# Performance work log

Hardware: AMD Instinct MI355X
Metric: run time of the kernel (lower is better)

Reference implementation:

```python
import jax, jax.numpy as jnp
import numpy as np

E, B, T = 8, 8, 1024
DIN = 640    # hidden_state_dim + conf_dim
DH = 1024    # 2 * hidden_state_dim
DOUT = 128   # 1024 // num_experts (slicing=True)
CODE = 256
TAU = 0.1
IMPORTANCE_REG = 0.01
EPS = 1e-8


def setup_inputs() -> dict:
    key = jax.random.key(0)
    ks = jax.random.split(key, 9)
    h = jax.random.normal(ks[0], (B, T, DIN), jnp.float32)
    code_emb = jax.random.normal(ks[1], (B, T, CODE), jnp.float32)
    u = jax.random.uniform(ks[2], (B, T, E), jnp.float32, 1e-6, 1.0 - 1e-6)
    gumbel_noise = -jnp.log(-jnp.log(u))
    code_anchor = jax.random.normal(ks[3], (E, CODE), jnp.float32)
    feature_importance = jax.random.normal(ks[4], (E, DIN), jnp.float32)
    W1 = jax.random.normal(ks[5], (E, DIN, DH), jnp.float32) * 0.02
    b1 = jax.random.normal(ks[6], (E, DH), jnp.float32) * 0.02
    W2 = jax.random.normal(ks[7], (E, DH, DOUT), jnp.float32) * 0.02
    b2 = jax.random.normal(ks[8], (E, DOUT), jnp.float32) * 0.02
    return {"h": h, "code_emb": code_emb, "gumbel_noise": gumbel_noise,
            "code_anchor": code_anchor, "feature_importance": feature_importance,
            "W1": W1, "b1": b1, "W2": W2, "b2": b2}


def _l2norm(x, axis):
    n = jnp.sqrt(jnp.sum(x * x, axis=axis, keepdims=True))
    return x / jnp.maximum(n, 1e-12)


def reference(h, code_emb, gumbel_noise, code_anchor, feature_importance, W1, b1, W2, b2):
    # router logits: cosine similarity between code_emb and code anchors  [B,T,E]
    anchor_n = _l2norm(code_anchor, axis=1)
    code_n = _l2norm(code_emb, axis=-1)
    router_logits = jnp.einsum('btd,ed->bte', code_n, anchor_n)
    # gumbel-softmax, tau=0.1, hard=False (noise provided for determinism)
    expert_weights = jax.nn.softmax((router_logits + gumbel_noise) / TAU, axis=-1)  # [B,T,E]
    # temperature-scaled importance softmax; importance_temperature=0.5, clamp no-op
    temp = jnp.clip(jnp.float32(0.5), 0.1, 5.0)
    importance = jax.nn.softmax(feature_importance / temp, axis=1)  # [E,DIN]
    # per-expert importance-weighted inputs [B,E,T,DIN]
    weighted_h = h[:, None, :, :] * importance[None, :, None, :]
    # all experts as one batched 2-layer MLP (exact GELU like torch nn.GELU)
    hid = jax.nn.gelu(jnp.einsum('betd,edh->beth', weighted_h, W1) + b1[None, :, None, :],
                      approximate=False)
    expert_outputs = jnp.einsum('beth,eho->beto', hid, W2) + b2[None, :, None, :]  # [B,E,T,DOUT]
    # slicing combine: expert i fills output slice [i*DOUT:(i+1)*DOUT], scaled by its gate
    gated = expert_outputs.transpose(0, 2, 1, 3) * expert_weights[..., None]  # [B,T,E,DOUT]
    full_output = gated.reshape(B, T, E * DOUT)  # [B,T,1024]
    # routing aux loss
    expert_counts = expert_weights.sum(0)  # [T,E]
    expert_load = expert_counts / (expert_counts.sum() + EPS)
    routing_loss = 0.5 * (jnp.std(expert_counts, ddof=1)
                          + (-expert_load * jnp.log(expert_load + EPS)).sum())
    imp_entropy = -(importance * jnp.log(importance + EPS)).sum(-1)  # [E]
    aux_loss = routing_loss + IMPORTANCE_REG * imp_entropy.mean()
    # diversity loss on raw feature_importance
    sim = feature_importance @ feature_importance.T  # [E,E]
    off = sim * (1.0 - jnp.eye(E, dtype=sim.dtype))
    diversity_loss = (off ** 2).sum() / (E * (E - 1))
    imp_mean = importance.mean(-1)
    imp_std = jnp.std(importance, axis=-1, ddof=1)
    return full_output, aux_loss, diversity_loss, imp_entropy, imp_mean, imp_std
```

## Files before the change

### kernel.cpp

```cpp
#include <hip/hip_runtime.h>
#include <math.h>

#define DIN 640
#define DH 1024
#define DOUT 128
#define CODEDIM 256
#define NE 8
#define NB 8
#define NT 1024
#define NTOK 8192
#define TAU_INV 10.0f
#define FEPS 1e-8f

#define AUX_OFF  8388608
#define DIV_OFF  8388609
#define ENT_OFF  8388610
#define MEAN_OFF 8388618
#define STD_OFF  8388626

typedef __bf16 bf16;
typedef bf16 bf16x8 __attribute__((ext_vector_type(8)));
typedef float f32x4 __attribute__((ext_vector_type(4)));

__device__ __forceinline__ float gelu(float x) {
  return 0.5f * x * (1.0f + erff(x * 0.70710678118654752f));
}

#define BAR() do { asm volatile("" ::: "memory"); __builtin_amdgcn_s_barrier(); asm volatile("" ::: "memory"); } while(0)
#define VMCNT5 asm volatile("s_waitcnt vmcnt(5)" ::: "memory")
#define VMCNT6 asm volatile("s_waitcnt vmcnt(6)" ::: "memory")
#define VMCNT0 asm volatile("s_waitcnt vmcnt(0)" ::: "memory")

__device__ __forceinline__ void gload16(const void* g, void* l) {
  __builtin_amdgcn_global_load_lds(
      (const __attribute__((address_space(1))) unsigned int*)g,
      (__attribute__((address_space(3))) unsigned int*)l, 16, 0, 0);
}

__device__ __forceinline__ float blk_sum(float v, float* sb) {
  #pragma unroll
  for (int o = 32; o > 0; o >>= 1) v += __shfl_down(v, o, 64);
  __syncthreads();
  if ((threadIdx.x & 63) == 0) sb[threadIdx.x >> 6] = v;
  __syncthreads();
  float tot = 0.f;
  int nw = blockDim.x >> 6;
  for (int i = 0; i < nw; ++i) tot += sb[i];
  return tot;
}

__device__ __forceinline__ float blk_max(float v, float* sb) {
  #pragma unroll
  for (int o = 32; o > 0; o >>= 1) v = fmaxf(v, __shfl_down(v, o, 64));
  __syncthreads();
  if ((threadIdx.x & 63) == 0) sb[threadIdx.x >> 6] = v;
  __syncthreads();
  float m = -3.0e38f;
  int nw = blockDim.x >> 6;
  for (int i = 0; i < nw; ++i) m = fmaxf(m, sb[i]);
  return m;
}

__global__ void k_imp(const float* __restrict__ fi, float* __restrict__ imp,
                      float* __restrict__ out) {
  __shared__ float sb[8];
  int e = blockIdx.x, tid = threadIdx.x;
  int d2v = tid + 512;
  float v0 = fi[e*DIN + tid] * 2.0f;
  float v1 = fi[e*DIN + tid + 256] * 2.0f;
  float v2 = (d2v < DIN) ? fi[e*DIN + d2v] * 2.0f : -3.0e38f;
  float m = blk_max(fmaxf(v0, fmaxf(v1, v2)), sb);
  float e0 = expf(v0 - m), e1 = expf(v1 - m);
  float e2 = (d2v < DIN) ? expf(v2 - m) : 0.f;
  float s = blk_sum(e0 + e1 + e2, sb);
  float inv = 1.0f / s;
  float p0 = e0*inv, p1 = e1*inv, p2 = e2*inv;
  imp[e*DIN + tid] = p0;
  imp[e*DIN + tid + 256] = p1;
  if (d2v < DIN) imp[e*DIN + d2v] = p2;
  float ok2 = (d2v < DIN) ? 1.f : 0.f;
  float sp  = p0 + p1 + ok2*p2;
  float sp2 = p0*p0 + p1*p1 + ok2*p2*p2;
  float se  = p0*logf(p0 + FEPS) + p1*logf(p1 + FEPS) + ok2*p2*logf(p2 + FEPS);
  sp  = blk_sum(sp, sb);
  sp2 = blk_sum(sp2, sb);
  se  = blk_sum(se, sb);
  if (tid == 0) {
    out[ENT_OFF + e]  = -se;
    out[MEAN_OFF + e] = sp * (1.0f/DIN);
    float var = (sp2 - sp*sp*(1.0f/DIN)) * (1.0f/(DIN-1));
    out[STD_OFF + e]  = sqrtf(fmaxf(var, 0.f));
  }
}

__global__ void k_anchor_div(const float* __restrict__ ca, const float* __restrict__ fi,
                             float* __restrict__ anch, float* __restrict__ out) {
  __shared__ float sb[8];
  __shared__ float sd[256];
  int tid = threadIdx.x;
  for (int e = 0; e < NE; ++e) {
    float x = ca[e*CODEDIM + tid];
    float ss = blk_sum(x*x, sb);
    anch[e*CODEDIM + tid] = x / fmaxf(sqrtf(ss), 1e-12f);
  }
  int p = tid >> 2, q = tid & 3;
  int i = p >> 3, j = p & 7;
  float dot = 0.f;
  for (int d = q*160; d < q*160 + 160; ++d) dot += fi[i*DIN + d] * fi[j*DIN + d];
  sd[tid] = dot;
  __syncthreads();
  if (tid < 64) {
    float s = sd[tid*4] + sd[tid*4+1] + sd[tid*4+2] + sd[tid*4+3];
    int ii = tid >> 3, jj = tid & 7;
    float val = (ii != jj) ? s*s : 0.f;
    #pragma unroll
    for (int o = 32; o > 0; o >>= 1) val += __shfl_down(val, o, 64);
    if (tid == 0) out[DIV_OFF] = val * (1.0f/56.0f);
  }
}

__global__ void k_transpose(const float* __restrict__ src, bf16* __restrict__ dst,
                            int R, int C, const float* __restrict__ scale) {
  __shared__ float tile[64][65];
  int c0 = blockIdx.x*64, r0 = blockIdx.y*64;
  int ee = blockIdx.z;
  const float* s = src + (size_t)ee*R*C;
  bf16* d = dst + (size_t)ee*C*R;
  int tx = threadIdx.x & 63, ty = threadIdx.x >> 6;
  #pragma unroll
  for (int p = 0; p < 16; ++p) {
    int r = p*4 + ty;
    tile[r][tx] = s[(size_t)(r0 + r)*C + c0 + tx];
  }
  __syncthreads();
  float sc = scale ? scale[(size_t)ee*R + r0 + tx] : 1.0f;
  #pragma unroll
  for (int p = 0; p < 16; ++p) {
    int cr = p*4 + ty;
    d[(size_t)(c0 + cr)*R + r0 + tx] = (bf16)(tile[tx][cr] * sc);
  }
}

__global__ void k_h2b(const float* __restrict__ h, bf16* __restrict__ xb) {
  size_t i = (size_t)blockIdx.x*256 + threadIdx.x;
  const float4* p = (const float4*)(h + i*8);
  float4 v0 = p[0], v1 = p[1];
  bf16x8 o;
  o[0]=(bf16)v0.x; o[1]=(bf16)v0.y; o[2]=(bf16)v0.z; o[3]=(bf16)v0.w;
  o[4]=(bf16)v1.x; o[5]=(bf16)v1.y; o[6]=(bf16)v1.z; o[7]=(bf16)v1.w;
  *(bf16x8*)(xb + i*8) = o;
}

__global__ void k_router(const float* __restrict__ ce, const float* __restrict__ gn,
                         const float* __restrict__ anch, float* __restrict__ ew) {
  __shared__ float anc[NE*CODEDIM];
  int tid = threadIdx.x;
  for (int i2 = tid; i2 < NE*CODEDIM; i2 += 256) anc[i2] = anch[i2];
  __syncthreads();
  int wv = tid >> 6, lane = tid & 63;
  int token = blockIdx.x*4 + wv;
  float4 x = *(const float4*)(ce + (size_t)token*CODEDIM + lane*4);
  float ss = x.x*x.x + x.y*x.y + x.z*x.z + x.w*x.w;
  #pragma unroll
  for (int o = 1; o < 64; o <<= 1) ss += __shfl_xor(ss, o, 64);
  float inv = 1.0f / fmaxf(sqrtf(ss), 1e-12f);
  const float* g = gn + (size_t)token*NE;
  float z[8];
  float m = -3.0e38f;
  #pragma unroll
  for (int e2 = 0; e2 < NE; ++e2) {
    const float* a = anc + e2*CODEDIM + lane*4;
    float d = x.x*a[0] + x.y*a[1] + x.z*a[2] + x.w*a[3];
    #pragma unroll
    for (int o = 1; o < 64; o <<= 1) d += __shfl_xor(d, o, 64);
    z[e2] = (d*inv + g[e2]) * TAU_INV;
    m = fmaxf(m, z[e2]);
  }
  float ssum = 0.f;
  float pz[8];
  #pragma unroll
  for (int e2 = 0; e2 < NE; ++e2) { pz[e2] = expf(z[e2] - m); ssum += pz[e2]; }
  float num = 0.f;
  #pragma unroll
  for (int e2 = 0; e2 < NE; ++e2) num = (lane == e2) ? pz[e2] : num;
  if (lane < NE) ew[(size_t)token*NE + lane] = num / ssum;
}

__global__ __launch_bounds__(256, 3)
void k_g1(const bf16* __restrict__ xb, const bf16* __restrict__ w1t,
          const float* __restrict__ b1, bf16* __restrict__ Hb, int ebase) {
  __shared__ __align__(16) char L[40960];
  const int bid = blockIdx.x;
  const int el = bid & 3, e = ebase + el;
  const int nt = (bid >> 2) & 3, mt = bid >> 4;
  const int M0 = mt * 64, N0 = nt * 256;
  const int tid = threadIdx.x;
  const int lane = tid & 63, w = tid >> 6;
  const int l15 = lane & 15, g4 = lane >> 4;
  const int nb = w * 64;

  unsigned pA = (unsigned)(w*1024 + lane*16);
  unsigned qA = pA ^ (((pA >> 7) & 3u) << 4);
  const char* gAsrc = (const char*)xb + (size_t)(M0 + (int)(qA >> 6))*(DIN*2) + (qA & 63u);
  const char* gBsrc[4];
  #pragma unroll
  for (int j = 0; j < 4; ++j) {
    unsigned p = (unsigned)((w*4 + j)*1024 + lane*16);
    unsigned q = p ^ (((p >> 7) & 3u) << 4);
    gBsrc[j] = (const char*)w1t + (size_t)(e*DH + N0 + (int)(q >> 6))*(DIN*2) + (q & 63u);
  }
  auto STAGE = [&](int buf, int t) {
    size_t ko = (size_t)t * 64;
    gload16(gAsrc + ko, L + buf*4096 + w*1024);
    #pragma unroll
    for (int j = 0; j < 4; ++j)
      gload16(gBsrc[j] + ko, L + 8192 + buf*16384 + (w*4 + j)*1024);
  };

  unsigned afOff[4], bfOff[4];
  #pragma unroll
  for (int mi = 0; mi < 4; ++mi) {
    int row = mi*16 + l15;
    afOff[mi] = (unsigned)(row*64 + ((g4 ^ ((row >> 1) & 3)) << 4));
  }
  #pragma unroll
  for (int ni = 0; ni < 4; ++ni) {
    int row = nb + ni*16 + l15;
    bfOff[ni] = (unsigned)(row*64 + ((g4 ^ ((row >> 1) & 3)) << 4));
  }

  f32x4 acc[4][4] = {};
  STAGE(0, 0);
  for (int t = 0; t < 20; ++t) {
    int buf = t & 1;
    if (t < 19) { STAGE(buf ^ 1, t + 1); VMCNT5; } else { VMCNT0; }
    BAR();
    const char* Ab = L + buf*4096;
    const char* Bb = L + 8192 + buf*16384;
    bf16x8 af[4], bfr[4];
    #pragma unroll
    for (int mi = 0; mi < 4; ++mi) af[mi] = *(const bf16x8*)(Ab + afOff[mi]);
    #pragma unroll
    for (int ni = 0; ni < 4; ++ni) bfr[ni] = *(const bf16x8*)(Bb + bfOff[ni]);
    #pragma unroll
    for (int mi = 0; mi < 4; ++mi)
      #pragma unroll
      for (int ni = 0; ni < 4; ++ni)
        acc[mi][ni] = __builtin_amdgcn_mfma_f32_16x16x32_bf16(
            af[mi], bfr[ni], acc[mi][ni], 0, 0, 0);
    BAR();
  }
  __syncthreads();
  float b1v[4];
  #pragma unroll
  for (int ni = 0; ni < 4; ++ni)
    b1v[ni] = b1[e*DH + N0 + nb + ni*16 + l15];
  #pragma unroll
  for (int mi = 0; mi < 4; ++mi)
    #pragma unroll
    for (int ni = 0; ni < 4; ++ni)
      #pragma unroll
      for (int r = 0; r < 4; ++r) {
        float v = gelu(acc[mi][ni][r] + b1v[ni]);
        int row = mi*16 + g4*4 + r;
        int col = nb + ni*16 + l15;
        *(bf16*)(L + row*520 + col*2) = (bf16)v;
      }
  __syncthreads();
  #pragma unroll
  for (int j = 0; j < 8; ++j) {
    int c = j*256 + tid;
    int row = c >> 5, slot = c & 31;
    bf16x8 v = *(const bf16x8*)(L + row*520 + slot*16);
    *(bf16x8*)((char*)Hb + (size_t)(el*NTOK + M0 + row)*(DH*2) + (size_t)N0*2 + slot*16) = v;
  }
}

__global__ __launch_bounds__(256, 3)
void k_g2(const bf16* __restrict__ Hb, const bf16* __restrict__ w2t,
          const float* __restrict__ b2, const float* __restrict__ ew,
          float* __restrict__ out, int ebase) {
  __shared__ __align__(16) char L[49152];
  const int bid = blockIdx.x;
  const int el = bid & 3, e = ebase + el;
  const int mt = bid >> 2;
  const int M0 = mt * 64;
  const int tid = threadIdx.x;
  const int lane = tid & 63, w = tid >> 6;
  const int l15 = lane & 15, g4 = lane >> 4;
  const int nb = w * 32;

  const char* gAsrc[2];
  #pragma unroll
  for (int j = 0; j < 2; ++j) {
    unsigned p = (unsigned)((w*2 + j)*1024 + lane*16);
    unsigned q = p ^ (((p >> 7) & 7u) << 4);
    gAsrc[j] = (const char*)Hb + (size_t)(el*NTOK + M0 + (int)(q >> 7))*(DH*2) + (q & 127u);
  }
  const char* gBsrc[4];
  #pragma unroll
  for (int j = 0; j < 4; ++j) {
    unsigned p = (unsigned)((w*4 + j)*1024 + lane*16);
    unsigned q = p ^ (((p >> 7) & 7u) << 4);
    gBsrc[j] = (const char*)w2t + (size_t)(e*DOUT + (int)(q >> 7))*(DH*2) + (q & 127u);
  }
  auto STAGE = [&](int buf, int t) {
    size_t ko = (size_t)t * 128;
    #pragma unroll
    for (int j = 0; j < 2; ++j)
      gload16(gAsrc[j] + ko, L + buf*8192 + (w*2 + j)*1024);
    #pragma unroll
    for (int j = 0; j < 4; ++j)
      gload16(gBsrc[j] + ko, L + 16384 + buf*16384 + (w*4 + j)*1024);
  };

  unsigned afOff[4][2], bfOff[2][2];
  #pragma unroll
  for (int mi = 0; mi < 4; ++mi)
    #pragma unroll
    for (int kk = 0; kk < 2; ++kk) {
      int row = mi*16 + l15;
      int slot = kk*4 + g4;
      afOff[mi][kk] = (unsigned)(row*128 + ((slot ^ (row & 7)) << 4));
    }
  #pragma unroll
  for (int ni = 0; ni < 2; ++ni)
    #pragma unroll
    for (int kk = 0; kk < 2; ++kk) {
      int row = nb + ni*16 + l15;
      int slot = kk*4 + g4;
      bfOff[ni][kk] = (unsigned)(row*128 + ((slot ^ (row & 7)) << 4));
    }

  f32x4 acc[4][2] = {};
  STAGE(0, 0);
  for (int t = 0; t < 16; ++t) {
    int buf = t & 1;
    if (t < 15) { STAGE(buf ^ 1, t + 1); VMCNT6; } else { VMCNT0; }
    BAR();
    const char* Ab = L + buf*8192;
    const char* Bb = L + 16384 + buf*16384;
    #pragma unroll
    for (int kk = 0; kk < 2; ++kk) {
      bf16x8 af[4], bfr[2];
      #pragma unroll
      for (int mi = 0; mi < 4; ++mi) af[mi] = *(const bf16x8*)(Ab + afOff[mi][kk]);
      #pragma unroll
      for (int ni = 0; ni < 2; ++ni) bfr[ni] = *(const bf16x8*)(Bb + bfOff[ni][kk]);
      #pragma unroll
      for (int mi = 0; mi < 4; ++mi)
        #pragma unroll
        for (int ni = 0; ni < 2; ++ni)
          acc[mi][ni] = __builtin_amdgcn_mfma_f32_16x16x32_bf16(
              af[mi], bfr[ni], acc[mi][ni], 0, 0, 0);
    }
    BAR();
  }
  float b2v[2];
  #pragma unroll
  for (int ni = 0; ni < 2; ++ni)
    b2v[ni] = b2[e*DOUT + nb + ni*16 + l15];
  float gt[4][4];
  #pragma unroll
  for (int mi = 0; mi < 4; ++mi)
    #pragma unroll
    for (int r = 0; r < 4; ++r)
      gt[mi][r] = ew[(size_t)(M0 + mi*16 + g4*4 + r)*NE + e];
  #pragma unroll
  for (int mi = 0; mi < 4; ++mi)
    #pragma unroll
    for (int ni = 0; ni < 2; ++ni)
      #pragma unroll
      for (int r = 0; r < 4; ++r) {
        int tok = M0 + mi*16 + g4*4 + r;
        int o = nb + ni*16 + l15;
        out[(size_t)tok*(NE*DOUT) + e*DOUT + o] = (acc[mi][ni][r] + b2v[ni]) * gt[mi][r];
      }
}

__global__ void k_counts(const float* __restrict__ ew, float* __restrict__ counts,
                         float* __restrict__ partials) {
  __shared__ float sb[4];
  int g2 = blockIdx.x*256 + threadIdx.x;
  float c = 0.f;
  #pragma unroll
  for (int b = 0; b < NB; ++b) c += ew[b*(NT*NE) + g2];
  counts[g2] = c;
  float tot = blk_sum(c, sb);
  if (threadIdx.x == 0) partials[blockIdx.x] = tot;
}

__global__ void k_aux(const float* __restrict__ counts, const float* __restrict__ partials,
                      float* __restrict__ out) {
  __shared__ float sb[4];
  int tid = threadIdx.x;
  float pv = (tid < 32) ? partials[tid] : 0.f;
  float total = blk_sum(pv, sb);
  float invt = 1.0f / (total + FEPS);
  float sq = 0.f, ent = 0.f;
  for (int i2 = tid; i2 < NT*NE; i2 += 256) {
    float c = counts[i2];
    sq += c*c;
    float ld = c * invt;
    ent -= ld * logf(ld + FEPS);
  }
  sq = blk_sum(sq, sb);
  ent = blk_sum(ent, sb);
  if (tid == 0) {
    float var = (sq - total*total*(1.0f/(NT*NE))) * (1.0f/(NT*NE - 1));
    float stdv = sqrtf(fmaxf(var, 0.f));
    float ment = 0.f;
    #pragma unroll
    for (int e2 = 0; e2 < NE; ++e2) ment += out[ENT_OFF + e2];
    ment *= (1.0f/NE);
    out[AUX_OFF] = 0.5f*(stdv + ent) + 0.01f*ment;
  }
}

extern "C" void kernel_launch(void* const* d_in, const int* in_sizes, int n_in,
                              void* d_out, int out_size, void* d_ws, size_t ws_size,
                              hipStream_t stream) {
  const float* h  = (const float*)d_in[0];
  const float* ce = (const float*)d_in[1];
  const float* gn = (const float*)d_in[2];
  const float* ca = (const float*)d_in[3];
  const float* fi = (const float*)d_in[4];
  const float* W1 = (const float*)d_in[5];
  const float* b1 = (const float*)d_in[6];
  const float* W2 = (const float*)d_in[7];
  const float* b2 = (const float*)d_in[8];
  float* out = (float*)d_out;
  char* ws = (char*)d_ws;
  bf16*  w1t      = (bf16*)(ws);
  bf16*  w2t      = (bf16*)(ws + 10485760);
  bf16*  xbuf     = (bf16*)(ws + 12582912);
  float* imp      = (float*)(ws + 23068672);
  float* anch     = (float*)(ws + 23089152);
  float* ew       = (float*)(ws + 23097344);
  float* counts   = (float*)(ws + 23359488);
  float* partials = (float*)(ws + 23392256);
  bf16*  Hbuf     = (bf16*)(ws + 23396352);

  k_imp<<<dim3(8), dim3(256), 0, stream>>>(fi, imp, out);
  k_anchor_div<<<dim3(1), dim3(256), 0, stream>>>(ca, fi, anch, out);
  k_transpose<<<dim3(16, 10, 8), dim3(256), 0, stream>>>(W1, w1t, 640, 1024, imp);
  k_transpose<<<dim3(2, 16, 8), dim3(256), 0, stream>>>(W2, w2t, 1024, 128, nullptr);
  k_h2b<<<dim3(2560), dim3(256), 0, stream>>>(h, xbuf);
  k_router<<<dim3(2048), dim3(256), 0, stream>>>(ce, gn, anch, ew);
  k_g1<<<dim3(2048), dim3(256), 0, stream>>>(xbuf, w1t, b1, Hbuf, 0);
  k_g2<<<dim3(512), dim3(256), 0, stream>>>(Hbuf, w2t, b2, ew, out, 0);
  k_g1<<<dim3(2048), dim3(256), 0, stream>>>(xbuf, w1t, b1, Hbuf, 4);
  k_g2<<<dim3(512), dim3(256), 0, stream>>>(Hbuf, w2t, b2, ew, out, 4);
  k_counts<<<dim3(32), dim3(256), 0, stream>>>(ew, counts, partials);
  k_aux<<<dim3(1), dim3(256), 0, stream>>>(counts, partials, out);
}
```

Baseline: 234.3 us.

## Retile first-layer GEMM to 128x128 tiles with K=64 single-buffered stages

New measurement: 202.2 us. 13.7% less time.

```diff
diff --git a/kernel.cpp b/kernel.cpp
--- a/kernel.cpp
+++ b/kernel.cpp
@@ -27,7 +27,6 @@
 }
 
 #define BAR() do { asm volatile("" ::: "memory"); __builtin_amdgcn_s_barrier(); asm volatile("" ::: "memory"); } while(0)
-#define VMCNT5 asm volatile("s_waitcnt vmcnt(5)" ::: "memory")
 #define VMCNT6 asm volatile("s_waitcnt vmcnt(6)" ::: "memory")
 #define VMCNT0 asm volatile("s_waitcnt vmcnt(0)" ::: "memory")
 
@@ -186,75 +185,79 @@
   if (lane < NE) ew[(size_t)token*NE + lane] = num / ssum;
 }
 
+#define G1_LDS 34816
 __global__ __launch_bounds__(256, 3)
 void k_g1(const bf16* __restrict__ xb, const bf16* __restrict__ w1t,
           const float* __restrict__ b1, bf16* __restrict__ Hb, int ebase) {
-  __shared__ __align__(16) char L[40960];
+  __shared__ __align__(16) char L[G1_LDS];
   const int bid = blockIdx.x;
   const int el = bid & 3, e = ebase + el;
-  const int nt = (bid >> 2) & 3, mt = bid >> 4;
-  const int M0 = mt * 64, N0 = nt * 256;
+  const int nt = (bid >> 2) & 7, mt = bid >> 5;
+  const int M0 = mt * 128, N0 = nt * 128;
   const int tid = threadIdx.x;
   const int lane = tid & 63, w = tid >> 6;
   const int l15 = lane & 15, g4 = lane >> 4;
-  const int nb = w * 64;
-
-  unsigned pA = (unsigned)(w*1024 + lane*16);
-  unsigned qA = pA ^ (((pA >> 7) & 3u) << 4);
-  const char* gAsrc = (const char*)xb + (size_t)(M0 + (int)(qA >> 6))*(DIN*2) + (qA & 63u);
+  const int wr = w >> 1, wc = w & 1;
+
+  const char* gAsrc[4];
   const char* gBsrc[4];
   #pragma unroll
   for (int j = 0; j < 4; ++j) {
     unsigned p = (unsigned)((w*4 + j)*1024 + lane*16);
-    unsigned q = p ^ (((p >> 7) & 3u) << 4);
-    gBsrc[j] = (const char*)w1t + (size_t)(e*DH + N0 + (int)(q >> 6))*(DIN*2) + (q & 63u);
-  }
-  auto STAGE = [&](int buf, int t) {
-    size_t ko = (size_t)t * 64;
-    gload16(gAsrc + ko, L + buf*4096 + w*1024);
-    #pragma unroll
-    for (int j = 0; j < 4; ++j)
-      gload16(gBsrc[j] + ko, L + 8192 + buf*16384 + (w*4 + j)*1024);
-  };
-
-  unsigned afOff[4], bfOff[4];
-  #pragma unroll
-  for (int mi = 0; mi < 4; ++mi) {
-    int row = mi*16 + l15;
-    afOff[mi] = (unsigned)(row*64 + ((g4 ^ ((row >> 1) & 3)) << 4));
-  }
-  #pragma unroll
-  for (int ni = 0; ni < 4; ++ni) {
-    int row = nb + ni*16 + l15;
-    bfOff[ni] = (unsigned)(row*64 + ((g4 ^ ((row >> 1) & 3)) << 4));
-  }
+    unsigned q = p ^ (((p >> 7) & 7u) << 4);
+    gAsrc[j] = (const char*)xb + (size_t)(M0 + (int)(q >> 7))*(DIN*2) + (q & 127u);
+    gBsrc[j] = (const char*)w1t + (size_t)(e*DH + N0 + (int)(q >> 7))*(DIN*2) + (q & 127u);
+  }
+
+  unsigned afOff[4][2], bfOff[4][2];
+  #pragma unroll
+  for (int mi = 0; mi < 4; ++mi)
+    #pragma unroll
+    for (int kk = 0; kk < 2; ++kk) {
+      int row = wr*64 + mi*16 + l15;
+      int slot = kk*4 + g4;
+      afOff[mi][kk] = (unsigned)(row*128 + ((slot ^ (row & 7)) << 4));
+    }
+  #pragma unroll
+  for (int ni = 0; ni < 4; ++ni)
+    #pragma unroll
+    for (int kk = 0; kk < 2; ++kk) {
+      int row = wc*64 + ni*16 + l15;
+      int slot = kk*4 + g4;
+      bfOff[ni][kk] = (unsigned)(16384 + row*128 + ((slot ^ (row & 7)) << 4));
+    }
 
   f32x4 acc[4][4] = {};
-  STAGE(0, 0);
-  for (int t = 0; t < 20; ++t) {
-    int buf = t & 1;
-    if (t < 19) { STAGE(buf ^ 1, t + 1); VMCNT5; } else { VMCNT0; }
+  for (int t = 0; t < 10; ++t) {
+    if (t) BAR();
+    size_t ko = (size_t)t * 128;
+    #pragma unroll
+    for (int j = 0; j < 4; ++j) {
+      gload16(gAsrc[j] + ko, L + (w*4 + j)*1024);
+      gload16(gBsrc[j] + ko, L + 16384 + (w*4 + j)*1024);
+    }
+    VMCNT0;
     BAR();
-    const char* Ab = L + buf*4096;
-    const char* Bb = L + 8192 + buf*16384;
-    bf16x8 af[4], bfr[4];
-    #pragma unroll
-    for (int mi = 0; mi < 4; ++mi) af[mi] = *(const bf16x8*)(Ab + afOff[mi]);
-    #pragma unroll
-    for (int ni = 0; ni < 4; ++ni) bfr[ni] = *(const bf16x8*)(Bb + bfOff[ni]);
-    #pragma unroll
-    for (int mi = 0; mi < 4; ++mi)
-      #pragma unroll
-      for (int ni = 0; ni < 4; ++ni)
-        acc[mi][ni] = __builtin_amdgcn_mfma_f32_16x16x32_bf16(
-            af[mi], bfr[ni], acc[mi][ni], 0, 0, 0);
-    BAR();
-  }
-  __syncthreads();
+    #pragma unroll
+    for (int kk = 0; kk < 2; ++kk) {
+      bf16x8 af[4], bfr[4];
+      #pragma unroll
+      for (int mi = 0; mi < 4; ++mi) af[mi] = *(const bf16x8*)(L + afOff[mi][kk]);
+      #pragma unroll
+      for (int ni = 0; ni < 4; ++ni) bfr[ni] = *(const bf16x8*)(L + bfOff[ni][kk]);
+      #pragma unroll
+      for (int mi = 0; mi < 4; ++mi)
+        #pragma unroll
+        for (int ni = 0; ni < 4; ++ni)
+          acc[mi][ni] = __builtin_amdgcn_mfma_f32_16x16x32_bf16(
+              af[mi], bfr[ni], acc[mi][ni], 0, 0, 0);
+    }
+  }
+  BAR();
   float b1v[4];
   #pragma unroll
   for (int ni = 0; ni < 4; ++ni)
-    b1v[ni] = b1[e*DH + N0 + nb + ni*16 + l15];
+    b1v[ni] = b1[e*DH + N0 + wc*64 + ni*16 + l15];
   #pragma unroll
   for (int mi = 0; mi < 4; ++mi)
     #pragma unroll
@@ -262,16 +265,16 @@
       #pragma unroll
       for (int r = 0; r < 4; ++r) {
         float v = gelu(acc[mi][ni][r] + b1v[ni]);
-        int row = mi*16 + g4*4 + r;
-        int col = nb + ni*16 + l15;
-        *(bf16*)(L + row*520 + col*2) = (bf16)v;
+        int row = wr*64 + mi*16 + g4*4 + r;
+        int col = wc*64 + ni*16 + l15;
+        *(bf16*)(L + row*272 + col*2) = (bf16)v;
       }
   __syncthreads();
   #pragma unroll
   for (int j = 0; j < 8; ++j) {
     int c = j*256 + tid;
-    int row = c >> 5, slot = c & 31;
-    bf16x8 v = *(const bf16x8*)(L + row*520 + slot*16);
+    int row = c >> 4, slot = c & 15;
+    bf16x8 v = *(const bf16x8*)(L + row*272 + slot*16);
     *(bf16x8*)((char*)Hb + (size_t)(el*NTOK + M0 + row)*(DH*2) + (size_t)N0*2 + slot*16) = v;
   }
 }
```
